# Performance work log

Measured on AMD Instinct MI355X. Metric: run time of the kernel, lower is better.

Reference implementation:

```python
import jax, jax.numpy as jnp
import numpy as np

N_BLADES = 8

def _build_cayley():
    """Geometric-product table for Cl(3,0): C[i,j,k] s.t. (e_i * e_j) = sum_k C[i,j,k] e_k.
    Blade order: [1, e1, e2, e3, e12, e13, e23, e123] via bitmasks [0,1,2,4,3,5,6,7]."""
    blades = [0, 1, 2, 4, 3, 5, 6, 7]
    idx = {b: i for i, b in enumerate(blades)}
    C = np.zeros((8, 8, 8), dtype=np.float32)
    for i, a in enumerate(blades):
        for j, b in enumerate(blades):
            aa = a >> 1
            cnt = 0
            while aa:
                cnt += bin(aa & b).count('1')
                aa >>= 1
            sign = -1.0 if (cnt & 1) else 1.0
            C[i, j, idx[a ^ b]] += sign
    return jnp.asarray(C)

CAYLEY = _build_cayley()

def clifford_linear(x, w, b):
    # x: (..., 8), w: (8,), b: (8,) -> geometric product w * x + b
    return jnp.einsum('ijk,i,...j->...k', CAYLEY, w, x) + b

def setup_inputs() -> dict:
    key = jax.random.key(0)
    ks = jax.random.split(key, 9)
    B, S = 4, 4096
    inp = {'x': jax.random.normal(ks[0], (B, S, N_BLADES), dtype=jnp.float32)}
    names = ['wq', 'bq', 'wk', 'bk', 'wv', 'bv', 'wo', 'bo']
    for i, n in enumerate(names):
        scale = 1.0 / np.sqrt(N_BLADES) if n.startswith('w') else 0.02
        inp[n] = jax.random.normal(ks[i + 1], (N_BLADES,), dtype=jnp.float32) * scale
    return inp

def reference(x, wq, bq, wk, bk, wv, bv, wo, bo):
    # head_dim = max(1, 8 // 2) = 4 -> scale = sqrt(4) = 2
    scale = jnp.float32(2.0)
    Q = clifford_linear(x, wq, bq)  # (B,S,8)
    K = clifford_linear(x, wk, bk)
    V = clifford_linear(x, wv, bv)
    c0 = CAYLEY[..., 0]  # (8,8) scalar part of geometric product
    attn = jnp.einsum('ij,bsi,btj->bst', c0, Q, K) / scale  # (B,S,S)
    attn = jax.nn.softmax(attn, axis=-1)
    out = jnp.einsum('bst,btk->bsk', attn, V)  # (B,S,8)
    return clifford_linear(out, wo, bo)
```

## Files before the change

kernel.cpp:

```cpp
#include <hip/hip_runtime.h>
#include <math.h>

#define SEQ 4096
#define NBATCH 4
#define SGRP 32
#define TWAVES 8
#define TCHUNK (SEQ / TWAVES)
#define TT 32

typedef _Float16 f16;
typedef __attribute__((ext_vector_type(8))) _Float16 f16x8;
typedef __attribute__((ext_vector_type(8))) __bf16 bf16x8;
typedef __attribute__((ext_vector_type(16))) float f32x16;
typedef __attribute__((ext_vector_type(4))) unsigned u32x4;
typedef __attribute__((ext_vector_type(2))) unsigned u32x2;

__device__ __forceinline__ float fexp2(float x) {
#if __has_builtin(__builtin_amdgcn_exp2f)
  return __builtin_amdgcn_exp2f(x);
#else
  return exp2f(x);
#endif
}

__device__ __forceinline__ u32x2 pswap(unsigned a, unsigned b) {
#if __has_builtin(__builtin_amdgcn_permlane32_swap)
  return __builtin_amdgcn_permlane32_swap(a, b, false, false);
#else
  asm volatile("v_permlane32_swap_b32 %0, %1" : "+v"(a), "+v"(b));
  u32x2 r; r[0] = a; r[1] = b; return r;
#endif
}

__device__ __forceinline__ unsigned exp2_pk_bf16(float a, float b) {
  unsigned e0 = __builtin_bit_cast(unsigned, fexp2(a));
  unsigned e1 = __builtin_bit_cast(unsigned, fexp2(b));
  return __builtin_amdgcn_perm(e1, e0, 0x07060302u);
}

__device__ __forceinline__ unsigned short f2bf(float f) {
  unsigned u = __builtin_bit_cast(unsigned, f);
  u += 0x7FFF + ((u >> 16) & 1);
  return (unsigned short)(u >> 16);
}

__device__ __forceinline__ float cl_sign(int amask, int bmask) {
  int cnt = 0, aa = amask >> 1;
  while (aa) { cnt += __popc(aa & bmask); aa >>= 1; }
  return (cnt & 1) ? -1.f : 1.f;
}

__global__ __launch_bounds__(128) void ck_qkv(const float* __restrict__ x,
                                              const float* __restrict__ wq,
                                              const float* __restrict__ bq,
                                              const float* __restrict__ wk,
                                              const float* __restrict__ bk,
                                              const float* __restrict__ wv,
                                              const float* __restrict__ bv,
                                              f16* __restrict__ Qp,
                                              f16* __restrict__ Kp,
                                              unsigned short* __restrict__ Vt) {
  __shared__ float Pl[288];
  const int blades[8] = {0, 1, 2, 4, 3, 5, 6, 7};
  int tid = threadIdx.x;

  if (tid < 64) {
    int j = tid >> 3, k = tid & 7;
    int bj = blades[j];
    float mq = 0.f, mk = 0.f, mv = 0.f;
    for (int i = 0; i < 8; ++i) {
      int ai = blades[i];
      if (blades[ai ^ bj] != k) continue;
      float sgn = cl_sign(ai, bj);
      mq += sgn * wq[i]; mk += sgn * wk[i]; mv += sgn * wv[i];
    }
    float c0 = cl_sign(blades[k], blades[k]);
    const float F = 0.72134752044448170368f;
    Pl[tid]       = mq * c0 * F;
    Pl[64 + tid]  = mk;
    Pl[128 + tid] = mv;
    if (j == 0) {
      Pl[256 + k] = bq[k] * c0 * F;
      Pl[264 + k] = bk[k];
      Pl[272 + k] = bv[k];
    }
  }
  __syncthreads();

  int row = blockIdx.x * 128 + tid;
  int b = row >> 12;
  int s = row & (SEQ - 1);
  const float4* x4 = (const float4*)(x + (size_t)row * 8);
  float4 xa = x4[0], xb = x4[1];
  float xr[8] = {xa.x, xa.y, xa.z, xa.w, xb.x, xb.y, xb.z, xb.w};
  float q[8], k[8], v[8];
#pragma unroll
  for (int c = 0; c < 8; ++c) { q[c] = Pl[256 + c]; k[c] = Pl[264 + c]; v[c] = Pl[272 + c]; }
#pragma unroll
  for (int j = 0; j < 8; ++j) {
    float xj = xr[j];
#pragma unroll
    for (int c = 0; c < 8; ++c) {
      q[c] = fmaf(xj, Pl[j * 8 + c], q[c]);
      k[c] = fmaf(xj, Pl[64 + j * 8 + c], k[c]);
      v[c] = fmaf(xj, Pl[128 + j * 8 + c], v[c]);
    }
  }
  f16x8 qa, qb, ka;
#pragma unroll
  for (int c = 0; c < 8; ++c) {
    f16 h = (f16)q[c];
    qa[c] = h;
    qb[c] = (f16)(q[c] - (float)h);
    ka[c] = (f16)k[c];
  }
  f16x8* qrow = (f16x8*)(Qp + (size_t)row * 16);
  qrow[0] = qa; qrow[1] = qb;
  *(f16x8*)(Kp + (size_t)row * 8) = ka;
  unsigned short* vtb = Vt + (size_t)b * 9 * SEQ;
#pragma unroll
  for (int c = 0; c < 8; ++c) vtb[c * SEQ + s] = f2bf(v[c]);
  vtb[8 * SEQ + s] = 0x3F80;
}

__global__ __launch_bounds__(512, 4) void ck_attn(const f16* __restrict__ Qp,
                                                  const f16* __restrict__ Kp,
                                                  const unsigned short* __restrict__ Vt,
                                                  const float* __restrict__ wo,
                                                  const float* __restrict__ bo,
                                                  float* __restrict__ out) {
  __shared__ float Lo[TWAVES][SGRP][9];
  __shared__ float MoL[72];

  const int tid = threadIdx.x;
  const int w = tid >> 6;
  const int lane = tid & 63;
  const int ls = lane & 31;
  const int hf = lane >> 5;
  const int rowbase = blockIdx.x * SGRP;
  const int b = rowbase >> 12;

  if (tid < 64) {
    const int blades[8] = {0, 1, 2, 4, 3, 5, 6, 7};
    int j = tid >> 3, k = tid & 7;
    int bj = blades[j];
    float mo = 0.f;
    for (int i = 0; i < 8; ++i) {
      int ai = blades[i];
      if (blades[ai ^ bj] != k) continue;
      mo += cl_sign(ai, bj) * wo[i];
    }
    MoL[tid] = mo;
    if (j == 0) MoL[64 + k] = bo[k];
  }

  f16x8 qf = *(const f16x8*)(Qp + (size_t)(rowbase + ls) * 16 + 8 * hf);

  f32x16 accA = {0.f, 0.f, 0.f, 0.f, 0.f, 0.f, 0.f, 0.f,
                 0.f, 0.f, 0.f, 0.f, 0.f, 0.f, 0.f, 0.f};
  f32x16 accB = accA;
  const f32x16 zero = accA;

  const f16* kbase = Kp + ((size_t)b * SEQ + w * TCHUNK + ls) * 8;
  const unsigned short* vrow =
      Vt + ((size_t)b * 9 + (ls <= 8 ? ls : 8)) * SEQ + w * TCHUNK + 8 * hf;

  const int NIT = TCHUNK / TT;

#pragma unroll 1
  for (int it = 0; it < NIT; it += 2) {
    const int t0 = it * TT;
    f16x8 kfA = *(const f16x8*)(kbase + (size_t)t0 * 8);
    f16x8 kfB = *(const f16x8*)(kbase + (size_t)(t0 + TT) * 8);
    u32x4 vA0 = *(const u32x4*)(vrow + t0);
    u32x4 vA1 = *(const u32x4*)(vrow + t0 + 16);
    u32x4 vB0 = *(const u32x4*)(vrow + t0 + TT);
    u32x4 vB1 = *(const u32x4*)(vrow + t0 + TT + 16);

    f32x16 sA = __builtin_amdgcn_mfma_f32_32x32x16_f16(kfA, qf, zero, 0, 0, 0);
    f32x16 sB = __builtin_amdgcn_mfma_f32_32x32x16_f16(kfB, qf, zero, 0, 0, 0);

    {
      unsigned d0 = exp2_pk_bf16(sA[0], sA[1]);
      unsigned d1 = exp2_pk_bf16(sA[2], sA[3]);
      unsigned d2 = exp2_pk_bf16(sA[4], sA[5]);
      unsigned d3 = exp2_pk_bf16(sA[6], sA[7]);
      u32x2 r02 = pswap(d0, d2);
      u32x2 r13 = pswap(d1, d3);
      u32x4 pb0 = {r02[0], r13[0], r02[1], r13[1]};
      accA = __builtin_amdgcn_mfma_f32_32x32x16_bf16(
          __builtin_bit_cast(bf16x8, vA0), __builtin_bit_cast(bf16x8, pb0), accA, 0, 0, 0);
      unsigned d4 = exp2_pk_bf16(sA[8], sA[9]);
      unsigned d5 = exp2_pk_bf16(sA[10], sA[11]);
      unsigned d6 = exp2_pk_bf16(sA[12], sA[13]);
      unsigned d7 = exp2_pk_bf16(sA[14], sA[15]);
      u32x2 r46 = pswap(d4, d6);
      u32x2 r57 = pswap(d5, d7);
      u32x4 pb1 = {r46[0], r57[0], r46[1], r57[1]};
      accA = __builtin_amdgcn_mfma_f32_32x32x16_bf16(
          __builtin_bit_cast(bf16x8, vA1), __builtin_bit_cast(bf16x8, pb1), accA, 0, 0, 0);
    }
    {
      unsigned d0 = exp2_pk_bf16(sB[0], sB[1]);
      unsigned d1 = exp2_pk_bf16(sB[2], sB[3]);
      unsigned d2 = exp2_pk_bf16(sB[4], sB[5]);
      unsigned d3 = exp2_pk_bf16(sB[6], sB[7]);
      u32x2 r02 = pswap(d0, d2);
      u32x2 r13 = pswap(d1, d3);
      u32x4 pb0 = {r02[0], r13[0], r02[1], r13[1]};
      accB = __builtin_amdgcn_mfma_f32_32x32x16_bf16(
          __builtin_bit_cast(bf16x8, vB0), __builtin_bit_cast(bf16x8, pb0), accB, 0, 0, 0);
      unsigned d4 = exp2_pk_bf16(sB[8], sB[9]);
      unsigned d5 = exp2_pk_bf16(sB[10], sB[11]);
      unsigned d6 = exp2_pk_bf16(sB[12], sB[13]);
      unsigned d7 = exp2_pk_bf16(sB[14], sB[15]);
      u32x2 r46 = pswap(d4, d6);
      u32x2 r57 = pswap(d5, d7);
      u32x4 pb1 = {r46[0], r57[0], r46[1], r57[1]};
      accB = __builtin_amdgcn_mfma_f32_32x32x16_bf16(
          __builtin_bit_cast(bf16x8, vB1), __builtin_bit_cast(bf16x8, pb1), accB, 0, 0, 0);
    }
  }

  if (hf == 0) {
    Lo[w][ls][0] = accA[0] + accB[0]; Lo[w][ls][1] = accA[1] + accB[1];
    Lo[w][ls][2] = accA[2] + accB[2]; Lo[w][ls][3] = accA[3] + accB[3];
    Lo[w][ls][8] = accA[4] + accB[4];
  } else {
    Lo[w][ls][4] = accA[0] + accB[0]; Lo[w][ls][5] = accA[1] + accB[1];
    Lo[w][ls][6] = accA[2] + accB[2]; Lo[w][ls][7] = accA[3] + accB[3];
  }
  __syncthreads();

  if (tid < SGRP * 9) {
    int s = tid / 9, j = tid - s * 9;
    float sum = 0.f;
#pragma unroll
    for (int w2 = 0; w2 < TWAVES; ++w2) sum += Lo[w2][s][j];
    Lo[0][s][j] = sum;
  }
  __syncthreads();

  if (tid < SGRP * 8) {
    int s = tid >> 3, ko = tid & 7;
    float inv = 1.f / Lo[0][s][8];
    float a = MoL[64 + ko];
#pragma unroll
    for (int j = 0; j < 8; ++j) a = fmaf(Lo[0][s][j] * inv, MoL[j * 8 + ko], a);
    out[(size_t)(rowbase + s) * 8 + ko] = a;
  }
}

extern "C" void kernel_launch(void* const* d_in, const int* in_sizes, int n_in,
                              void* d_out, int out_size, void* d_ws, size_t ws_size,
                              hipStream_t stream) {
  const float* x  = (const float*)d_in[0];
  const float* wq = (const float*)d_in[1];
  const float* bq = (const float*)d_in[2];
  const float* wk = (const float*)d_in[3];
  const float* bk = (const float*)d_in[4];
  const float* wv = (const float*)d_in[5];
  const float* bv = (const float*)d_in[6];
  const float* wo = (const float*)d_in[7];
  const float* bo = (const float*)d_in[8];

  f16* Qp = (f16*)d_ws;
  f16* Kp = Qp + (size_t)NBATCH * SEQ * 16;
  unsigned short* Vt = (unsigned short*)(Kp + (size_t)NBATCH * SEQ * 8);
  float* outp = (float*)d_out;

  hipLaunchKernelGGL(ck_qkv, dim3(NBATCH * SEQ / 128), dim3(128), 0, stream,
                     x, wq, bq, wk, bk, wv, bv, Qp, Kp, Vt);
  hipLaunchKernelGGL(ck_attn, dim3(NBATCH * SEQ / SGRP), dim3(512), 0, stream,
                     Qp, Kp, Vt, wo, bo, outp);
}
```

Before: 21.67 us.

## Split QKV projection across three block kinds and add MFMA priority hints

The QKV projection kernel now launches three times as many blocks, and each block computes only one of Q, K or V for its 128 rows. This raises parallelism for the small prologue kernel and cuts per-thread register and LDS use, at the cost of reading x three times. The attention loop is unrolled by two and wrapped in s_setprio hints so the MFMA and exp section gets higher wave priority.

New measurement: 22.46 us. 3.7% more time.

```diff
diff --git a/kernel.cpp b/kernel.cpp
--- a/kernel.cpp
+++ b/kernel.cpp
@@ -60,67 +60,71 @@
                                               f16* __restrict__ Qp,
                                               f16* __restrict__ Kp,
                                               unsigned short* __restrict__ Vt) {
-  __shared__ float Pl[288];
+  __shared__ float Pl[72];
   const int blades[8] = {0, 1, 2, 4, 3, 5, 6, 7};
-  int tid = threadIdx.x;
+  const int tid = threadIdx.x;
+  const int kind = blockIdx.x % 3;
+  const int row = (blockIdx.x / 3) * 128 + tid;
+
+  const float* wv_ = (kind == 0) ? wq : (kind == 1) ? wk : wv;
+  const float* bv_ = (kind == 0) ? bq : (kind == 1) ? bk : bv;
+  const float F = 0.72134752044448170368f;
 
   if (tid < 64) {
     int j = tid >> 3, k = tid & 7;
     int bj = blades[j];
-    float mq = 0.f, mk = 0.f, mv = 0.f;
+    float m = 0.f;
     for (int i = 0; i < 8; ++i) {
       int ai = blades[i];
       if (blades[ai ^ bj] != k) continue;
-      float sgn = cl_sign(ai, bj);
-      mq += sgn * wq[i]; mk += sgn * wk[i]; mv += sgn * wv[i];
-    }
-    float c0 = cl_sign(blades[k], blades[k]);
-    const float F = 0.72134752044448170368f;
-    Pl[tid]       = mq * c0 * F;
-    Pl[64 + tid]  = mk;
-    Pl[128 + tid] = mv;
+      m += cl_sign(ai, bj) * wv_[i];
+    }
+    if (kind == 0) m *= cl_sign(blades[k], blades[k]) * F;
+    Pl[tid] = m;
     if (j == 0) {
-      Pl[256 + k] = bq[k] * c0 * F;
-      Pl[264 + k] = bk[k];
-      Pl[272 + k] = bv[k];
+      float bb = bv_[k];
+      if (kind == 0) bb *= cl_sign(blades[k], blades[k]) * F;
+      Pl[64 + k] = bb;
     }
   }
   __syncthreads();
 
-  int row = blockIdx.x * 128 + tid;
-  int b = row >> 12;
-  int s = row & (SEQ - 1);
   const float4* x4 = (const float4*)(x + (size_t)row * 8);
   float4 xa = x4[0], xb = x4[1];
   float xr[8] = {xa.x, xa.y, xa.z, xa.w, xb.x, xb.y, xb.z, xb.w};
-  float q[8], k[8], v[8];
-#pragma unroll
-  for (int c = 0; c < 8; ++c) { q[c] = Pl[256 + c]; k[c] = Pl[264 + c]; v[c] = Pl[272 + c]; }
+  float y[8];
+#pragma unroll
+  for (int c = 0; c < 8; ++c) y[c] = Pl[64 + c];
 #pragma unroll
   for (int j = 0; j < 8; ++j) {
     float xj = xr[j];
 #pragma unroll
+    for (int c = 0; c < 8; ++c) y[c] = fmaf(xj, Pl[j * 8 + c], y[c]);
+  }
+
+  if (kind == 0) {
+    f16x8 qa, qb;
+#pragma unroll
     for (int c = 0; c < 8; ++c) {
-      q[c] = fmaf(xj, Pl[j * 8 + c], q[c]);
-      k[c] = fmaf(xj, Pl[64 + j * 8 + c], k[c]);
-      v[c] = fmaf(xj, Pl[128 + j * 8 + c], v[c]);
-    }
-  }
-  f16x8 qa, qb, ka;
-#pragma unroll
-  for (int c = 0; c < 8; ++c) {
-    f16 h = (f16)q[c];
-    qa[c] = h;
-    qb[c] = (f16)(q[c] - (float)h);
-    ka[c] = (f16)k[c];
-  }
-  f16x8* qrow = (f16x8*)(Qp + (size_t)row * 16);
-  qrow[0] = qa; qrow[1] = qb;
-  *(f16x8*)(Kp + (size_t)row * 8) = ka;
-  unsigned short* vtb = Vt + (size_t)b * 9 * SEQ;
-#pragma unroll
-  for (int c = 0; c < 8; ++c) vtb[c * SEQ + s] = f2bf(v[c]);
-  vtb[8 * SEQ + s] = 0x3F80;
+      f16 h = (f16)y[c];
+      qa[c] = h;
+      qb[c] = (f16)(y[c] - (float)h);
+    }
+    f16x8* qrow = (f16x8*)(Qp + (size_t)row * 16);
+    qrow[0] = qa; qrow[1] = qb;
+  } else if (kind == 1) {
+    f16x8 ka;
+#pragma unroll
+    for (int c = 0; c < 8; ++c) ka[c] = (f16)y[c];
+    *(f16x8*)(Kp + (size_t)row * 8) = ka;
+  } else {
+    int b = row >> 12;
+    int s = row & (SEQ - 1);
+    unsigned short* vtb = Vt + (size_t)b * 9 * SEQ;
+#pragma unroll
+    for (int c = 0; c < 8; ++c) vtb[c * SEQ + s] = f2bf(y[c]);
+    vtb[8 * SEQ + s] = 0x3F80;
+  }
 }
 
 __global__ __launch_bounds__(512, 4) void ck_attn(const f16* __restrict__ Qp,
@@ -167,7 +171,7 @@
 
   const int NIT = TCHUNK / TT;
 
-#pragma unroll 1
+#pragma unroll 2
   for (int it = 0; it < NIT; it += 2) {
     const int t0 = it * TT;
     f16x8 kfA = *(const f16x8*)(kbase + (size_t)t0 * 8);
@@ -177,6 +181,7 @@
     u32x4 vB0 = *(const u32x4*)(vrow + t0 + TT);
     u32x4 vB1 = *(const u32x4*)(vrow + t0 + TT + 16);
 
+    __builtin_amdgcn_s_setprio(1);
     f32x16 sA = __builtin_amdgcn_mfma_f32_32x32x16_f16(kfA, qf, zero, 0, 0, 0);
     f32x16 sB = __builtin_amdgcn_mfma_f32_32x32x16_f16(kfB, qf, zero, 0, 0, 0);
 
@@ -220,6 +225,7 @@
       accB = __builtin_amdgcn_mfma_f32_32x32x16_bf16(
           __builtin_bit_cast(bf16x8, vB1), __builtin_bit_cast(bf16x8, pb1), accB, 0, 0, 0);
     }
+    __builtin_amdgcn_s_setprio(0);
   }
 
   if (hf == 0) {
@@ -269,7 +275,7 @@
   unsigned short* Vt = (unsigned short*)(Kp + (size_t)NBATCH * SEQ * 8);
   float* outp = (float*)d_out;
 
-  hipLaunchKernelGGL(ck_qkv, dim3(NBATCH * SEQ / 128), dim3(128), 0, stream,
+  hipLaunchKernelGGL(ck_qkv, dim3(NBATCH * SEQ / 128 * 3), dim3(128), 0, stream,
                      x, wq, bq, wk, bk, wv, bv, Qp, Kp, Vt);
   hipLaunchKernelGGL(ck_attn, dim3(NBATCH * SEQ / SGRP), dim3(512), 0, stream,
                      Qp, Kp, Vt, wo, bo, outp);
```
